# Kernel tuning notes

Measured on AMD Instinct MI355X. Metric: run time of the kernel, lower is better.

## Reference

```python
import jax, jax.numpy as jnp
import numpy as np

B, N, D = 2, 4096, 256
H = 8
HD = D // H  # head dim = 32
DFF = 4 * D


def _layer_norm(x):
    # Matches source: (x - mean) / (std + 1e-6), std is population std (ddof=0)
    m = jnp.mean(x, axis=-1, keepdims=True)
    s = jnp.std(x, axis=-1, keepdims=True)
    return (x - m) / (s + 1e-6)


def setup_inputs() -> dict:
    key = jax.random.key(0)
    ks = jax.random.split(key, 11)
    sd = 1.0 / np.sqrt(D)
    sf = 1.0 / np.sqrt(DFF)
    return {
        "embeddings_in": jax.random.normal(ks[0], (B, N, D), dtype=jnp.float32),
        "Wq": jax.random.normal(ks[1], (D, D), dtype=jnp.float32) * sd,
        "bq": jnp.zeros((D,), dtype=jnp.float32),
        "Wk": jax.random.normal(ks[2], (D, D), dtype=jnp.float32) * sd,
        "bk": jnp.zeros((D,), dtype=jnp.float32),
        "Wv": jax.random.normal(ks[3], (D, D), dtype=jnp.float32) * sd,
        "bv": jnp.zeros((D,), dtype=jnp.float32),
        "Wo": jax.random.normal(ks[4], (D, D), dtype=jnp.float32) * sd,
        "bo": jnp.zeros((D,), dtype=jnp.float32),
        "W1": jax.random.normal(ks[5], (D, DFF), dtype=jnp.float32) * sd,
        "b1": jnp.zeros((DFF,), dtype=jnp.float32),
        "W2": jax.random.normal(ks[6], (DFF, D), dtype=jnp.float32) * sf,
        "b2": jnp.zeros((D,), dtype=jnp.float32),
    }


def reference(embeddings_in, Wq, bq, Wk, bk, Wv, bv, Wo, bo, W1, b1, W2, b2):
    x = embeddings_in
    xn1 = _layer_norm(x)
    # QKV projections, split into heads: [B,N,D] -> [B,H,N,HD]
    def heads(t):
        return jnp.transpose(t.reshape(B, N, H, HD), (0, 2, 1, 3))
    q = heads(xn1 @ Wq + bq)
    k = heads(xn1 @ Wk + bk)
    v = heads(xn1 @ Wv + bv)
    scores = jnp.einsum('bhnd,bhmd->bhnm', q, k) / jnp.sqrt(jnp.float32(HD))
    attn = jax.nn.softmax(scores, axis=-1)
    heads_out = jnp.einsum('bhnm,bhmd->bhnd', attn, v)
    attn_out = jnp.transpose(heads_out, (0, 2, 1, 3)).reshape(B, N, D)
    attn_out = attn_out @ Wo + bo  # dropout is identity in eval
    x_skip = attn_out + x
    xn2 = _layer_norm(x_skip)
    mlp = jax.nn.gelu(xn2 @ W1 + b1) @ W2 + b2
    return mlp + x_skip
```

## Files before the change

kernel.cpp:

```cpp
#include <hip/hip_runtime.h>
#include <hip/hip_bf16.h>

#define Bb 2
#define Nn 4096
#define Dd 256
#define Hh 8
#define HDh 32
#define DFFd 1024
#define MT (Bb*Nn)
#define Tt ((size_t)MT * Dd)
#define SPLIT 4
#define KVB (Nn / SPLIT)
#define NSTP (KVB / 64)

typedef __attribute__((ext_vector_type(8))) short short8;
typedef __attribute__((ext_vector_type(4))) float f32x4;
typedef __attribute__((address_space(1))) const unsigned int gu32;
typedef __attribute__((address_space(3))) unsigned int lu32;

__device__ __forceinline__ void gll16(const ushort* g, ushort* l) {
  __builtin_amdgcn_global_load_lds((gu32*)g, (lu32*)l, 16, 0, 0);
}
__device__ __forceinline__ float bf2f(ushort u){
  union { unsigned int i; float f; } v; v.i = ((unsigned int)u) << 16; return v.f;
}
__device__ __forceinline__ ushort f2bf(float f){
  union { float f; unsigned int i; } v; v.f = f;
  unsigned int r = v.i + 0x7fffu + ((v.i >> 16) & 1u);
  return (ushort)(r >> 16);
}
__device__ __forceinline__ int ars(int r){ return r * 64 + (r >> 3) * 32; }

__device__ __forceinline__ void ln_rows4(const float* __restrict__ x,
                                         ushort* __restrict__ out, int row0,
                                         int wave, int lane)
{
  #pragma unroll
  for (int r = 0; r < 4; r++) {
    const int row = row0 + wave * 4 + r;
    const float4 u = *(const float4*)(x + (size_t)row * Dd + lane * 4);
    float s1 = u.x + u.y + u.z + u.w;
    float s2 = u.x*u.x + u.y*u.y + u.z*u.z + u.w*u.w;
    #pragma unroll
    for (int m = 1; m < 64; m <<= 1) { s1 += __shfl_xor(s1, m, 64); s2 += __shfl_xor(s2, m, 64); }
    const float mean = s1 * (1.0f / Dd);
    float var = s2 * (1.0f / Dd) - mean * mean;
    var = var < 0.f ? 0.f : var;
    const float inv = 1.0f / (sqrtf(var) + 1e-6f);
    ushort4 o;
    o.x = f2bf((u.x - mean) * inv); o.y = f2bf((u.y - mean) * inv);
    o.z = f2bf((u.z - mean) * inv); o.w = f2bf((u.w - mean) * inv);
    *(ushort4*)(out + (size_t)row * Dd + lane * 4) = o;
  }
}

__global__ __launch_bounds__(256) void p0_kernel(
    const float* __restrict__ Wq, const float* __restrict__ Wk,
    const float* __restrict__ Wv, const float* __restrict__ Wo,
    const float* __restrict__ W1, const float* __restrict__ W2,
    const float* __restrict__ bq, const float* __restrict__ bk,
    const float* __restrict__ bv, ushort* __restrict__ wt,
    float* __restrict__ bqkv, const float* __restrict__ x,
    ushort* __restrict__ xn1)
{
  const int bid = blockIdx.x, t = threadIdx.x;
  __shared__ __align__(16) ushort T[64][72];
  if (bid < 192) {
    const float* src; ushort* dst; int Nsrc, Kdst, kt, nt;
    if (bid < 64) {
      const int m = bid >> 4, tile = bid & 15;
      kt = tile >> 2; nt = tile & 3; Nsrc = 256; Kdst = 256;
      src = (m == 0 ? Wq : m == 1 ? Wk : m == 2 ? Wv : Wo);
      dst = (m == 3) ? (wt + 196608) : (wt + m * 65536);
    } else if (bid < 128) {
      const int tile = bid - 64; kt = tile >> 4; nt = tile & 15;
      Nsrc = 1024; Kdst = 256; src = W1; dst = wt + 262144;
    } else {
      const int tile = bid - 128; kt = tile >> 2; nt = tile & 3;
      Nsrc = 256; Kdst = 1024; src = W2; dst = wt + 524288;
    }
    const int k0 = kt * 64, n0 = nt * 64;
    const int cc = t & 15, rr = t >> 4;
    #pragma unroll
    for (int pass = 0; pass < 4; pass++) {
      const int k = rr + pass * 16;
      const float4 v = *(const float4*)(src + (size_t)(k0 + k) * Nsrc + n0 + cc * 4);
      T[cc * 4 + 0][k] = f2bf(v.x); T[cc * 4 + 1][k] = f2bf(v.y);
      T[cc * 4 + 2][k] = f2bf(v.z); T[cc * 4 + 3][k] = f2bf(v.w);
    }
    __syncthreads();
    const int nl = t >> 2, ks = (t & 3) * 16;
    const short8 a = *(const short8*)(&T[nl][ks]);
    const short8 b = *(const short8*)(&T[nl][ks + 8]);
    ushort* drow = dst + (size_t)(n0 + nl) * Kdst + k0 + ks;
    *(short8*)(drow) = a; *(short8*)(drow + 8) = b;
  } else if (bid == 192) {
    bqkv[t] = bq[t]; bqkv[256 + t] = bk[t]; bqkv[512 + t] = bv[t];
  }
  ln_rows4(x, xn1, bid * 16, t >> 6, t & 63);
}

__global__ __launch_bounds__(256) void ln_kernel(const float* __restrict__ x,
                                                 ushort* __restrict__ out)
{
  ln_rows4(x, out, blockIdx.x * 16, threadIdx.x >> 6, threadIdx.x & 63);
}

template<int EPI, int BM>
__global__ __launch_bounds__(256) void gemm_epi(
    const ushort* __restrict__ A, const ushort* __restrict__ BT,
    const float* __restrict__ bias, const float* __restrict__ res,
    void* __restrict__ outv, int N, int K)
{
  constexpr int MI = BM / 64;
  constexpr int AI = BM / 32;
  __shared__ __align__(16) ushort AsF[2][BM * 64 + (BM / 8) * 32];
  __shared__ __align__(16) ushort BsF[2][64 * 64 + 8 * 32];
  const int tid = threadIdx.x;
  const int wave = tid >> 6, lane = tid & 63;
  const int quad = lane >> 4, l15 = lane & 15;
  const int n0 = blockIdx.x * 64, m0 = blockIdx.y * BM;
  f32x4 acc[MI][4];
  #pragma unroll
  for (int mt = 0; mt < MI; mt++)
    #pragma unroll
    for (int nt = 0; nt < 4; nt++) acc[mt][nt] = (f32x4){0.f,0.f,0.f,0.f};
  const int srow = lane >> 3, scol = (lane & 7) * 8;
  const ushort* gA[AI];
  #pragma unroll
  for (int ai = 0; ai < AI; ai++)
    gA[ai] = A + (size_t)(m0 + ai * 32 + wave * 8 + srow) * K + scol;
  const ushort* gB[2];
  #pragma unroll
  for (int bi = 0; bi < 2; bi++)
    gB[bi] = BT + (size_t)(n0 + bi * 32 + wave * 8 + srow) * K + scol;
  int aoff[MI], boff[4];
  #pragma unroll
  for (int mt = 0; mt < MI; mt++) aoff[mt] = ars(wave * 16 * MI + mt * 16 + l15);
  #pragma unroll
  for (int nt = 0; nt < 4; nt++) boff[nt] = ars(nt * 16 + l15);
  #pragma unroll
  for (int ai = 0; ai < AI; ai++) gll16(gA[ai], &AsF[0][ars(ai * 32 + wave * 8)]);
  #pragma unroll
  for (int bi = 0; bi < 2; bi++) gll16(gB[bi], &BsF[0][ars(bi * 32 + wave * 8)]);
  __syncthreads();
  const int NC = K >> 6;
  int p = 0;
  for (int c = 0; c < NC; c++) {
    if (c + 1 < NC) {
      #pragma unroll
      for (int ai = 0; ai < AI; ai++)
        gll16(gA[ai] + (c + 1) * 64, &AsF[p ^ 1][ars(ai * 32 + wave * 8)]);
      #pragma unroll
      for (int bi = 0; bi < 2; bi++)
        gll16(gB[bi] + (c + 1) * 64, &BsF[p ^ 1][ars(bi * 32 + wave * 8)]);
    }
    #pragma unroll
    for (int kk = 0; kk < 2; kk++) {
      short8 af[MI];
      #pragma unroll
      for (int mt = 0; mt < MI; mt++)
        af[mt] = *(const short8*)(&AsF[p][aoff[mt] + kk * 32 + quad * 8]);
      #pragma unroll
      for (int nt = 0; nt < 4; nt++) {
        const short8 bf = *(const short8*)(&BsF[p][boff[nt] + kk * 32 + quad * 8]);
        #pragma unroll
        for (int mt = 0; mt < MI; mt++)
          acc[mt][nt] = __builtin_amdgcn_mfma_f32_16x16x32_bf16(af[mt], bf, acc[mt][nt], 0, 0, 0);
      }
    }
    __syncthreads();
    p ^= 1;
  }
  #pragma unroll
  for (int mt = 0; mt < MI; mt++) {
    const int row0 = m0 + wave * (16 * MI) + mt * 16 + quad * 4;
    #pragma unroll
    for (int nt = 0; nt < 4; nt++) {
      const int col = n0 + nt * 16 + l15;
      const float bv = bias[col];
      float c[4];
      #pragma unroll
      for (int i = 0; i < 4; i++) c[i] = acc[mt][nt][i] + bv;
      if (EPI == 0) {
        ushort* qkv = (ushort*)outv;
        const int w = col >> 8, cd = col & 255;
        const int h = cd >> 5, hd = cd & 31;
        const int b = row0 >> 12, n = row0 & (Nn - 1);
        if (w < 2) {
          const float sc2 = (w == 0) ? (1.4426950408889634f * 0.17677669529663687f) : 1.0f;
          ushort* dst = qkv + (size_t)w * Tt + ((size_t)((b * Hh + h) * Nn) + n) * HDh + hd;
          #pragma unroll
          for (int i = 0; i < 4; i++) dst[(size_t)i * HDh] = f2bf(c[i] * sc2);
        } else {
          ushort4 pk;
          pk.x = f2bf(c[0]); pk.y = f2bf(c[1]); pk.z = f2bf(c[2]); pk.w = f2bf(c[3]);
          *(ushort4*)(qkv + 2 * Tt + ((size_t)((b * Hh + h) * HDh + hd)) * Nn + n) = pk;
        }
      } else if (EPI == 1) {
        float* out = (float*)outv;
        #pragma unroll
        for (int i = 0; i < 4; i++) {
          const size_t idx = (size_t)(row0 + i) * N + col;
          out[idx] = c[i] + res[idx];
        }
      } else {
        ushort* out = (ushort*)outv;
        #pragma unroll
        for (int i = 0; i < 4; i++) {
          const float t = tanhf(0.7978845608028654f * (c[i] + 0.044715f * c[i] * c[i] * c[i]));
          out[(size_t)(row0 + i) * N + col] = f2bf(0.5f * c[i] * (1.0f + t));
        }
      }
    }
  }
}

__global__ __launch_bounds__(256, 4) void attn_kernel(
    const ushort* __restrict__ qp, const ushort* __restrict__ kp,
    const ushort* __restrict__ vtg, ushort* __restrict__ op0,
    ushort* __restrict__ op123, float* __restrict__ lp)
{
  __shared__ __align__(16) ushort Ks[2][64][32];
  __shared__ __align__(16) ushort Vt[2][32][72];
  __shared__ __align__(16) ushort Ps[4][64][40];
  const int tid = threadIdx.x;
  const int wave = tid >> 6, lane = tid & 63;
  const int quad = lane >> 4, l15 = lane & 15;
  const int qtb = blockIdx.x, bh = blockIdx.y, sp = blockIdx.z;
  const size_t base = (size_t)bh * Nn * HDh;
  const int q0 = qtb * 256 + wave * 64;
  short8 qf[4];
  #pragma unroll
  for (int qt = 0; qt < 4; qt++)
    qf[qt] = *(const short8*)(qp + base + (size_t)(q0 + qt * 16 + l15) * HDh + quad * 8);
  const int kv0 = sp * KVB;
  const ushort* kg = kp + base + (size_t)(kv0 + wave * 16 + (lane >> 2)) * HDh + (lane & 3) * 8;
  const int vr = tid >> 3, vc = (tid & 7) * 8;
  const ushort* vg = vtg + base + (size_t)vr * Nn + kv0 + vc;
  ushort* psw = &Ps[wave][0][0];
  f32x4 o[2][4], ol[4];
  #pragma unroll
  for (int qt = 0; qt < 4; qt++) {
    o[0][qt] = (f32x4){0,0,0,0}; o[1][qt] = (f32x4){0,0,0,0};
    ol[qt] = (f32x4){0,0,0,0};
  }
  const short one = (short)0x3F80;
  const short8 ones = {one,one,one,one,one,one,one,one};
  const f32x4 zero4 = {0,0,0,0};
  gll16(kg, &Ks[0][wave * 16][0]);
  int4 vreg = *(const int4*)vg;
  *(int4*)(&Vt[0][vr][vc]) = vreg;
  vreg = *(const int4*)(vg + 64);
  __syncthreads();
  #pragma unroll 2
  for (int step = 0; step < NSTP; step++) {
    const int p = step & 1;
    if (step + 1 < NSTP) {
      gll16(kg + (size_t)(step + 1) * 64 * HDh, &Ks[p ^ 1][wave * 16][0]);
      *(int4*)(&Vt[p ^ 1][vr][vc]) = vreg;
    }
    if (step + 2 < NSTP) vreg = *(const int4*)(vg + (size_t)(step + 2) * 64);
    #pragma unroll
    for (int half = 0; half < 2; half++) {
      #pragma unroll
      for (int nt2 = 0; nt2 < 2; nt2++) {
        const int nt = half * 2 + nt2;
        const short8 kf = *(const short8*)(&Ks[p][nt * 16 + l15][quad * 8]);
        #pragma unroll
        for (int qt = 0; qt < 4; qt++) {
          const f32x4 s = __builtin_amdgcn_mfma_f32_16x16x32_bf16(kf, qf[qt], zero4, 0, 0, 0);
          const float p0 = __builtin_amdgcn_exp2f(s[0]);
          const float p1 = __builtin_amdgcn_exp2f(s[1]);
          const float p2 = __builtin_amdgcn_exp2f(s[2]);
          const float p3 = __builtin_amdgcn_exp2f(s[3]);
          uint2 pk;
          pk.x = __builtin_amdgcn_perm(__float_as_uint(p1),
                                       __float_as_uint(p0), 0x07060302u);
          pk.y = __builtin_amdgcn_perm(__float_as_uint(p3),
                                       __float_as_uint(p2), 0x07060302u);
          *(uint2*)(psw + (qt * 16 + l15) * 40 + nt2 * 16 + quad * 4) = pk;
        }
      }
      __builtin_amdgcn_wave_barrier();
      const short8 v0 = *(const short8*)(&Vt[p][l15][half * 32 + quad * 8]);
      const short8 v1 = *(const short8*)(&Vt[p][16 + l15][half * 32 + quad * 8]);
      #pragma unroll
      for (int qt = 0; qt < 4; qt++) {
        const short8 pb = *(const short8*)(psw + (qt * 16 + l15) * 40 + quad * 8);
        o[0][qt] = __builtin_amdgcn_mfma_f32_16x16x32_bf16(v0, pb, o[0][qt], 0, 0, 0);
        o[1][qt] = __builtin_amdgcn_mfma_f32_16x16x32_bf16(v1, pb, o[1][qt], 0, 0, 0);
        ol[qt]   = __builtin_amdgcn_mfma_f32_16x16x32_bf16(ones, pb, ol[qt], 0, 0, 0);
      }
      __builtin_amdgcn_wave_barrier();
    }
    __syncthreads();
  }
  lp[(size_t)sp * (16 * Nn) + (size_t)bh * Nn + q0 + lane] = ol[lane >> 4][0];
  ushort* ob = (sp == 0 ? op0 : op123 + (size_t)(sp - 1) * (16 * (size_t)Nn * HDh));
  #pragma unroll
  for (int pass = 0; pass < 2; pass++) {
    #pragma unroll
    for (int qt2 = 0; qt2 < 2; qt2++) {
      const int qt = pass * 2 + qt2;
      #pragma unroll
      for (int dt = 0; dt < 2; dt++) {
        ushort4 pk;
        pk.x = f2bf(o[dt][qt][0]); pk.y = f2bf(o[dt][qt][1]);
        pk.z = f2bf(o[dt][qt][2]); pk.w = f2bf(o[dt][qt][3]);
        *(ushort4*)(psw + (qt2 * 16 + l15) * 40 + dt * 16 + quad * 4) = pk;
      }
    }
    __builtin_amdgcn_wave_barrier();
    #pragma unroll
    for (int j = 0; j < 2; j++) {
      const int row = j * 16 + (lane >> 2);
      const short8 ov = *(const short8*)(psw + row * 40 + (lane & 3) * 8);
      const int q = q0 + pass * 32 + row;
      *(short8*)(ob + ((size_t)bh * Nn + q) * HDh + (lane & 3) * 8) = ov;
    }
    __builtin_amdgcn_wave_barrier();
  }
}

__global__ __launch_bounds__(256) void attn_combine(
    const ushort* __restrict__ op0, const ushort* __restrict__ op123,
    const float* __restrict__ lp, ushort* __restrict__ attn)
{
  const int idx = blockIdx.x * 256 + threadIdx.x;
  const int d8 = idx & 3, n = (idx >> 2) & (Nn - 1), bh = idx >> 14;
  const size_t ln = (size_t)bh * Nn + n;
  float l = 0.f;
  #pragma unroll
  for (int sp = 0; sp < SPLIT; sp++) l += lp[(size_t)sp * (16 * Nn) + ln];
  const float inv = 1.0f / l;
  float acc[8];
  #pragma unroll
  for (int k = 0; k < 8; k++) acc[k] = 0.f;
  const size_t qoff = ln * HDh + d8 * 8;
  #pragma unroll
  for (int sp = 0; sp < SPLIT; sp++) {
    const ushort* src = (sp == 0 ? op0 : op123 + (size_t)(sp - 1) * (16 * (size_t)Nn * HDh)) + qoff;
    const short8 u = *(const short8*)src;
    #pragma unroll
    for (int k = 0; k < 8; k++) acc[k] += bf2f((ushort)u[k]);
  }
  short8 ov;
  #pragma unroll
  for (int k = 0; k < 8; k++) ov[k] = (short)f2bf(acc[k] * inv);
  const int b = bh >> 3, h = bh & 7;
  *(short8*)(attn + ((size_t)(b * Nn + n)) * Dd + h * HDh + d8 * 8) = ov;
}

extern "C" void kernel_launch(void* const* d_in, const int* in_sizes, int n_in,
                              void* d_out, int out_size, void* d_ws, size_t ws_size,
                              hipStream_t stream)
{
  const float* x  = (const float*)d_in[0];
  const float* Wq = (const float*)d_in[1];
  const float* bq = (const float*)d_in[2];
  const float* Wk = (const float*)d_in[3];
  const float* bk = (const float*)d_in[4];
  const float* Wv = (const float*)d_in[5];
  const float* bv = (const float*)d_in[6];
  const float* Wo = (const float*)d_in[7];
  const float* bo = (const float*)d_in[8];
  const float* W1 = (const float*)d_in[9];
  const float* b1 = (const float*)d_in[10];
  const float* W2 = (const float*)d_in[11];
  const float* b2 = (const float*)d_in[12];

  char* ws = (char*)d_ws;
  ushort* wt    = (ushort*)ws;
  ushort* wtqkv = wt;
  ushort* wto   = wt + 196608;
  ushort* wt1   = wt + 262144;
  ushort* wt2   = wt + 524288;
  float*  bqkv  = (float*)(ws + 786432 * 2);
  ushort* s0    = (ushort*)(ws + 786432 * 2 + 4096);
  ushort* s1    = s0 + Tt;
  ushort* s2    = s1 + Tt;
  ushort* s3    = s2 + Tt;
  float*  xsk   = (float*)(s3 + Tt);
  ushort* xn2   = (ushort*)(xsk + Tt);
  ushort* xn1   = s0;
  ushort* hid   = s0;
  ushort* op0   = s0;
  ushort* op123 = (ushort*)xsk;
  float*  lp    = (float*)d_out;
  ushort* attnb = (ushort*)((char*)d_out + (4u << 20));
  float*  outp  = (float*)d_out;

  const dim3 blk(256);
  hipLaunchKernelGGL(p0_kernel, dim3(512), blk, 0, stream,
                     Wq, Wk, Wv, Wo, W1, W2, bq, bk, bv, wt, bqkv, x, xn1);
  hipLaunchKernelGGL((gemm_epi<0,128>), dim3(12, 64), blk, 0, stream,
                     xn1, wtqkv, bqkv, (const float*)nullptr, (void*)s1, 768, Dd);

  hipLaunchKernelGGL(attn_kernel, dim3(Nn / 256, Bb * Hh, SPLIT), blk, 0, stream,
                     s1, s2, s3, op0, op123, lp);
  hipLaunchKernelGGL(attn_combine, dim3((Bb * Hh * Nn * 4) / 256), blk, 0, stream,
                     op0, op123, lp, attnb);

  hipLaunchKernelGGL((gemm_epi<1,64>), dim3(4, 128), blk, 0, stream,
                     attnb, wto, bo, x, (void*)xsk, Dd, Dd);
  hipLaunchKernelGGL(ln_kernel, dim3(MT / 16), blk, 0, stream, xsk, xn2);
  hipLaunchKernelGGL((gemm_epi<2,128>), dim3(16, 64), blk, 0, stream,
                     xn2, wt1, b1, (const float*)nullptr, (void*)hid, DFFd, Dd);
  hipLaunchKernelGGL((gemm_epi<1,64>), dim3(4, 128), blk, 0, stream,
                     hid, wt2, b2, xsk, (void*)outp, Dd, DFFd);
}
```

Before: 197.8 us.

## Fuse split-KV attention combine into Wo GEMM and use bit-trick exp2

Removes the separate attn_combine kernel: the Wo projection GEMM now reads the four split-KV partial outputs and row sums directly, normalizes them, and stages the result as its A tile. Partial-output and row-sum buffers are reassigned within the workspace and output so none of them aliases xsk. Separately, the attention softmax exp2 is replaced with an integer bit-trick approximation (fma plus float-to-int conversion) that builds bf16 bit patterns directly. This saves a launch and an intermediate round trip, but the fused GEMM recomputes the combine for each of its four column blocks, and the exp approximation loses accuracy.

Result: slower. 203.2 us (+2.7%).

```diff
diff --git a/kernel.cpp b/kernel.cpp
--- a/kernel.cpp
+++ b/kernel.cpp
@@ -216,10 +216,93 @@
   }
 }
 
+__global__ __launch_bounds__(256) void wo_fused(
+    const ushort* __restrict__ op0, const ushort* __restrict__ op1,
+    const ushort* __restrict__ op2, const ushort* __restrict__ op3,
+    const float* __restrict__ lp, const ushort* __restrict__ BT,
+    const float* __restrict__ bias, const float* __restrict__ res,
+    float* __restrict__ out)
+{
+  __shared__ __align__(16) ushort AsF[2][64 * 64 + 8 * 32];
+  __shared__ __align__(16) ushort BsF[2][64 * 64 + 8 * 32];
+  const int tid = threadIdx.x;
+  const int wave = tid >> 6, lane = tid & 63;
+  const int quad = lane >> 4, l15 = lane & 15;
+  const int n0 = blockIdx.x * 64, m0 = blockIdx.y * 64;
+  f32x4 acc[4];
+  #pragma unroll
+  for (int nt = 0; nt < 4; nt++) acc[nt] = (f32x4){0.f,0.f,0.f,0.f};
+  const int srow = lane >> 3, scol = (lane & 7) * 8;
+  const int mrow[2] = { m0 + wave * 8 + srow, m0 + 32 + wave * 8 + srow };
+  const ushort* gB[2];
+  #pragma unroll
+  for (int bi = 0; bi < 2; bi++)
+    gB[bi] = BT + (size_t)(n0 + bi * 32 + wave * 8 + srow) * Dd + scol;
+  const int aoff = ars(wave * 16 + l15);
+  int boff[4];
+  #pragma unroll
+  for (int nt = 0; nt < 4; nt++) boff[nt] = ars(nt * 16 + l15);
+  auto combineA = [&](int c, int ai) -> short8 {
+    const int m = mrow[ai];
+    const int k = c * 64 + scol;
+    const int b = m >> 12, n = m & (Nn - 1);
+    const int bh = b * Hh + (k >> 5), hd = k & 31;
+    const size_t off = ((size_t)bh * Nn + n) * HDh + hd;
+    const short8 u0 = *(const short8*)(op0 + off);
+    const short8 u1 = *(const short8*)(op1 + off);
+    const short8 u2 = *(const short8*)(op2 + off);
+    const short8 u3 = *(const short8*)(op3 + off);
+    const size_t ln = (size_t)bh * Nn + n;
+    const float inv = 1.0f / (lp[ln] + lp[65536 + ln] + lp[131072 + ln] + lp[196608 + ln]);
+    short8 r;
+    #pragma unroll
+    for (int j = 0; j < 8; j++)
+      r[j] = (short)f2bf((bf2f((ushort)u0[j]) + bf2f((ushort)u1[j]) +
+                          bf2f((ushort)u2[j]) + bf2f((ushort)u3[j])) * inv);
+    return r;
+  };
+  short8 ar0 = combineA(0, 0), ar1 = combineA(0, 1);
+  gll16(gB[0], &BsF[0][ars(wave * 8)]);
+  gll16(gB[1], &BsF[0][ars(32 + wave * 8)]);
+  int p = 0;
+  for (int c = 0; c < 4; c++) {
+    *(short8*)(&AsF[p][ars(wave * 8 + srow) + scol])      = ar0;
+    *(short8*)(&AsF[p][ars(32 + wave * 8 + srow) + scol]) = ar1;
+    __syncthreads();
+    if (c + 1 < 4) {
+      gll16(gB[0] + (c + 1) * 64, &BsF[p ^ 1][ars(wave * 8)]);
+      gll16(gB[1] + (c + 1) * 64, &BsF[p ^ 1][ars(32 + wave * 8)]);
+      ar0 = combineA(c + 1, 0); ar1 = combineA(c + 1, 1);
+    }
+    #pragma unroll
+    for (int kk = 0; kk < 2; kk++) {
+      const short8 af = *(const short8*)(&AsF[p][aoff + kk * 32 + quad * 8]);
+      #pragma unroll
+      for (int nt = 0; nt < 4; nt++) {
+        const short8 bf = *(const short8*)(&BsF[p][boff[nt] + kk * 32 + quad * 8]);
+        acc[nt] = __builtin_amdgcn_mfma_f32_16x16x32_bf16(af, bf, acc[nt], 0, 0, 0);
+      }
+    }
+    p ^= 1;
+  }
+  const int row0 = m0 + wave * 16 + quad * 4;
+  #pragma unroll
+  for (int nt = 0; nt < 4; nt++) {
+    const int col = n0 + nt * 16 + l15;
+    const float bv = bias[col];
+    #pragma unroll
+    for (int i = 0; i < 4; i++) {
+      const size_t idx = (size_t)(row0 + i) * Dd + col;
+      out[idx] = acc[nt][i] + bv + res[idx];
+    }
+  }
+}
+
 __global__ __launch_bounds__(256, 4) void attn_kernel(
     const ushort* __restrict__ qp, const ushort* __restrict__ kp,
     const ushort* __restrict__ vtg, ushort* __restrict__ op0,
-    ushort* __restrict__ op123, float* __restrict__ lp)
+    ushort* __restrict__ op1, ushort* __restrict__ op2,
+    ushort* __restrict__ op3, float* __restrict__ lp)
 {
   __shared__ __align__(16) ushort Ks[2][64][32];
   __shared__ __align__(16) ushort Vt[2][32][72];
@@ -248,6 +331,8 @@
   const short one = (short)0x3F80;
   const short8 ones = {one,one,one,one,one,one,one,one};
   const f32x4 zero4 = {0,0,0,0};
+  const float SA = 8388608.0f;
+  const float SB = 1065102389.0f;
   gll16(kg, &Ks[0][wave * 16][0]);
   int4 vreg = *(const int4*)vg;
   *(int4*)(&Vt[0][vr][vc]) = vreg;
@@ -270,15 +355,13 @@
         #pragma unroll
         for (int qt = 0; qt < 4; qt++) {
           const f32x4 s = __builtin_amdgcn_mfma_f32_16x16x32_bf16(kf, qf[qt], zero4, 0, 0, 0);
-          const float p0 = __builtin_amdgcn_exp2f(s[0]);
-          const float p1 = __builtin_amdgcn_exp2f(s[1]);
-          const float p2 = __builtin_amdgcn_exp2f(s[2]);
-          const float p3 = __builtin_amdgcn_exp2f(s[3]);
+          const unsigned int i0 = (unsigned int)(int)fmaf(s[0], SA, SB);
+          const unsigned int i1 = (unsigned int)(int)fmaf(s[1], SA, SB);
+          const unsigned int i2 = (unsigned int)(int)fmaf(s[2], SA, SB);
+          const unsigned int i3 = (unsigned int)(int)fmaf(s[3], SA, SB);
           uint2 pk;
-          pk.x = __builtin_amdgcn_perm(__float_as_uint(p1),
-                                       __float_as_uint(p0), 0x07060302u);
-          pk.y = __builtin_amdgcn_perm(__float_as_uint(p3),
-                                       __float_as_uint(p2), 0x07060302u);
+          pk.x = __builtin_amdgcn_perm(i1, i0, 0x07060302u);
+          pk.y = __builtin_amdgcn_perm(i3, i2, 0x07060302u);
           *(uint2*)(psw + (qt * 16 + l15) * 40 + nt2 * 16 + quad * 4) = pk;
         }
       }
@@ -297,7 +380,7 @@
     __syncthreads();
   }
   lp[(size_t)sp * (16 * Nn) + (size_t)bh * Nn + q0 + lane] = ol[lane >> 4][0];
-  ushort* ob = (sp == 0 ? op0 : op123 + (size_t)(sp - 1) * (16 * (size_t)Nn * HDh));
+  ushort* ob = (sp == 0 ? op0 : sp == 1 ? op1 : sp == 2 ? op2 : op3);
   #pragma unroll
   for (int pass = 0; pass < 2; pass++) {
     #pragma unroll
@@ -321,35 +404,6 @@
     }
     __builtin_amdgcn_wave_barrier();
   }
-}
-
-__global__ __launch_bounds__(256) void attn_combine(
-    const ushort* __restrict__ op0, const ushort* __restrict__ op123,
-    const float* __restrict__ lp, ushort* __restrict__ attn)
-{
-  const int idx = blockIdx.x * 256 + threadIdx.x;
-  const int d8 = idx & 3, n = (idx >> 2) & (Nn - 1), bh = idx >> 14;
-  const size_t ln = (size_t)bh * Nn + n;
-  float l = 0.f;
-  #pragma unroll
-  for (int sp = 0; sp < SPLIT; sp++) l += lp[(size_t)sp * (16 * Nn) + ln];
-  const float inv = 1.0f / l;
-  float acc[8];
-  #pragma unroll
-  for (int k = 0; k < 8; k++) acc[k] = 0.f;
-  const size_t qoff = ln * HDh + d8 * 8;
-  #pragma unroll
-  for (int sp = 0; sp < SPLIT; sp++) {
-    const ushort* src = (sp == 0 ? op0 : op123 + (size_t)(sp - 1) * (16 * (size_t)Nn * HDh)) + qoff;
-    const short8 u = *(const short8*)src;
-    #pragma unroll
-    for (int k = 0; k < 8; k++) acc[k] += bf2f((ushort)u[k]);
-  }
-  short8 ov;
-  #pragma unroll
-  for (int k = 0; k < 8; k++) ov[k] = (short)f2bf(acc[k] * inv);
-  const int b = bh >> 3, h = bh & 7;
-  *(short8*)(attn + ((size_t)(b * Nn + n)) * Dd + h * HDh + d8 * 8) = ov;
 }
 
 extern "C" void kernel_launch(void* const* d_in, const int* in_sizes, int n_in,
@@ -383,12 +437,13 @@
   ushort* s3    = s2 + Tt;
   float*  xsk   = (float*)(s3 + Tt);
   ushort* xn2   = (ushort*)(xsk + Tt);
+  float*  lp    = (float*)(xn2 + Tt);
   ushort* xn1   = s0;
   ushort* hid   = s0;
   ushort* op0   = s0;
-  ushort* op123 = (ushort*)xsk;
-  float*  lp    = (float*)d_out;
-  ushort* attnb = (ushort*)((char*)d_out + (4u << 20));
+  ushort* op1   = xn2;
+  ushort* op2   = (ushort*)d_out;
+  ushort* op3   = (ushort*)d_out + Tt;
   float*  outp  = (float*)d_out;
 
   const dim3 blk(256);
@@ -398,12 +453,10 @@
                      xn1, wtqkv, bqkv, (const float*)nullptr, (void*)s1, 768, Dd);
 
   hipLaunchKernelGGL(attn_kernel, dim3(Nn / 256, Bb * Hh, SPLIT), blk, 0, stream,
-                     s1, s2, s3, op0, op123, lp);
-  hipLaunchKernelGGL(attn_combine, dim3((Bb * Hh * Nn * 4) / 256), blk, 0, stream,
-                     op0, op123, lp, attnb);
-
-  hipLaunchKernelGGL((gemm_epi<1,64>), dim3(4, 128), blk, 0, stream,
-                     attnb, wto, bo, x, (void*)xsk, Dd, Dd);
+                     s1, s2, s3, op0, op1, op2, op3, lp);
+
+  hipLaunchKernelGGL(wo_fused, dim3(4, 128), blk, 0, stream,
+                     op0, op1, op2, op3, lp, wto, bo, x, xsk);
   hipLaunchKernelGGL(ln_kernel, dim3(MT / 16), blk, 0, stream, xsk, xn2);
   hipLaunchKernelGGL((gemm_epi<2,128>), dim3(16, 64), blk, 0, stream,
                      xn2, wt1, b1, (const float*)nullptr, (void*)hid, DFFd, Dd);
```
